# Optimization experiments

Measured on AMD Instinct MI355X. Metric: run time of the kernel, lower is better.

The kernel has to match this reference:

```python
import jax, jax.numpy as jnp
import numpy as np

B, S, H = 1, 2048, 2048
NH, NKV, HD = 32, 4, 128
G = NH // NKV            # query groups per kv head
EPS = 1e-6
THETA = 1000000.0


def _rmsnorm(x, w):
    # per-head RMSNorm over last (head_dim) axis
    var = jnp.mean(jnp.square(x), axis=-1, keepdims=True)
    return x * jax.lax.rsqrt(var + EPS) * w


def _rotate_half(x):
    x1, x2 = jnp.split(x, 2, axis=-1)
    return jnp.concatenate([-x2, x1], axis=-1)


def _rope(x, cos, sin):
    # x: [B,S,h,HD], cos/sin: [S,HD]
    c = cos[None, :, None, :]
    s = sin[None, :, None, :]
    return x * c + _rotate_half(x) * s


def setup_inputs() -> dict:
    key = jax.random.key(0)
    ks = jax.random.split(key, 7)
    inv_freq = 1.0 / (THETA ** (jnp.arange(0, HD, 2, dtype=jnp.float32) / HD))
    freqs = jnp.outer(jnp.arange(S, dtype=jnp.float32), inv_freq)  # [S, HD/2]
    emb = jnp.concatenate([freqs, freqs], axis=-1)                 # [S, HD]
    std = 0.02
    return {
        "hidden_states": jax.random.normal(ks[0], (B, S, H), jnp.float32),
        "wq": jax.random.normal(ks[1], (H, NH * HD), jnp.float32) * std,
        "wk": jax.random.normal(ks[2], (H, NKV * HD), jnp.float32) * std,
        "wv": jax.random.normal(ks[3], (H, NKV * HD), jnp.float32) * std,
        "wo": jax.random.normal(ks[4], (NH * HD, H), jnp.float32) * std,
        "q_norm_w": jnp.ones((HD,), jnp.float32),
        "k_norm_w": jnp.ones((HD,), jnp.float32),
        "cos": jnp.cos(emb),
        "sin": jnp.sin(emb),
    }


def reference(hidden_states, wq, wk, wv, wo, q_norm_w, k_norm_w, cos, sin):
    b, s, _ = hidden_states.shape
    q = (hidden_states @ wq).reshape(b, s, NH, HD)
    k = (hidden_states @ wk).reshape(b, s, NKV, HD)
    v = (hidden_states @ wv).reshape(b, s, NKV, HD)
    # QK per-head RMSNorm, then interleaved RoPE (rotate-half form)
    q = _rope(_rmsnorm(q, q_norm_w), cos, sin)
    k = _rope(_rmsnorm(k, k_norm_w), cos, sin)
    # GQA: group Q heads per KV head instead of materializing repeated K/V
    qg = q.reshape(b, s, NKV, G, HD)
    scaling = HD ** -0.5
    scores = jnp.einsum('bqhgd,bkhd->bhgqk', qg, k) * scaling  # [B,NKV,G,S,S]
    causal = jnp.tril(jnp.ones((s, s), bool))
    scores = jnp.where(causal, scores, jnp.finfo(scores.dtype).min)
    p = jax.nn.softmax(scores, axis=-1)
    attn = jnp.einsum('bhgqk,bkhd->bqhgd', p, v).reshape(b, s, NH * HD)
    return attn @ wo
```

## Files before the change

### kernel.cpp

```cpp
#include <hip/hip_runtime.h>
#include <hip/hip_bf16.h>
#include <stdint.h>

#define SEQ 2048
#define HDIM 128
#define NHEADS 32
#define NKVH 4

typedef unsigned short u16;
typedef __bf16 bf16_t;
typedef bf16_t bf16x8 __attribute__((ext_vector_type(8)));
typedef float floatx4 __attribute__((ext_vector_type(4)));

__device__ __forceinline__ float bf2f(u16 u) {
  union { uint32_t i; float f; } v; v.i = ((uint32_t)u) << 16; return v.f;
}
__device__ __forceinline__ u16 f2bf(float f) {
  if (__builtin_isnan(f)) return 0;
  union { float f; uint32_t i; } v; v.f = f;
  uint32_t r = v.i + 0x7fffu + ((v.i >> 16) & 1u);
  return (u16)(r >> 16);
}
__device__ __forceinline__ float loadf_any(const void* p, size_t i, int isbf) {
  return isbf ? bf2f(((const u16*)p)[i]) : ((const float*)p)[i];
}

__device__ __forceinline__ void gload_lds16(const u16* g, u16* l) {
  __builtin_amdgcn_global_load_lds((__attribute__((address_space(1))) void*)g,
                                   (__attribute__((address_space(3))) void*)l,
                                   16, 0, 0);
}

__device__ __forceinline__ floatx4 mfma16(bf16x8 a, bf16x8 b, floatx4 c) {
  return __builtin_amdgcn_mfma_f32_16x16x32_bf16(a, b, c, 0, 0, 0);
}

struct InPack { const u16* p[9]; int n[9]; };

__global__ void detect_all(InPack pk, int* __restrict__ flags) {
  const int which = blockIdx.x;
  const u16* x = pk.p[which];
  const int n = pk.n[which];
  __shared__ int s_sane, s_zeven, s_zodd;
  if (threadIdx.x == 0) { s_sane = 0; s_zeven = 0; s_zodd = 0; }
  __syncthreads();
  const int ns = n < 8192 ? n : 8192;
  int sane = 0, zeven = 0, zodd = 0;
  for (int i = threadIdx.x; i < ns; i += 256) {
    const u16 u = x[i];
    const int e = (u >> 7) & 0xff;
    if ((e >= 96 && e <= 159) || u == 0) sane++;
    if (u == 0) { if (i & 1) zodd++; else zeven++; }
  }
#pragma unroll
  for (int off = 32; off >= 1; off >>= 1) {
    sane += __shfl_xor(sane, off, 64);
    zeven += __shfl_xor(zeven, off, 64);
    zodd += __shfl_xor(zodd, off, 64);
  }
  if ((threadIdx.x & 63) == 0) {
    atomicAdd(&s_sane, sane);
    atomicAdd(&s_zeven, zeven);
    atomicAdd(&s_zodd, zodd);
  }
  __syncthreads();
  if (threadIdx.x == 0) {
    const int even = (ns + 1) / 2, odd = ns / 2;
    const bool mostly_sane = (s_sane * 10 >= ns * 9);
    const bool fp32_const_pattern = (s_zeven * 2 >= even) && (s_zodd * 10 <= odd);
    flags[which] = (mostly_sane && !fp32_const_pattern) ? 1 : 0;
    if (which == 0) flags[15] = 1;
  }
}

__device__ __forceinline__ void transpose_tile(
    u16 (&tile)[64][65], const void* __restrict__ in, u16* __restrict__ out,
    int R, int C, int isbf, int bx, int by) {
  const int c0 = bx * 64, r0 = by * 64;
  const int t = threadIdx.x;
  const int tr = t >> 4;
  const int tc4 = (t & 15) * 4;
  if (isbf) {
#pragma unroll
    for (int i = 0; i < 4; i++) {
      const int r = i * 16 + tr;
      const ushort4 v = *(const ushort4*)((const u16*)in +
                                          (size_t)(r0 + r) * C + c0 + tc4);
      tile[r][tc4 + 0] = v.x; tile[r][tc4 + 1] = v.y;
      tile[r][tc4 + 2] = v.z; tile[r][tc4 + 3] = v.w;
    }
  } else {
#pragma unroll
    for (int i = 0; i < 4; i++) {
      const int r = i * 16 + tr;
      const float4 v = *(const float4*)((const float*)in +
                                        (size_t)(r0 + r) * C + c0 + tc4);
      tile[r][tc4 + 0] = f2bf(v.x); tile[r][tc4 + 1] = f2bf(v.y);
      tile[r][tc4 + 2] = f2bf(v.z); tile[r][tc4 + 3] = f2bf(v.w);
    }
  }
  __syncthreads();
#pragma unroll
  for (int j = 0; j < 4; j++) {
    const int cc = j * 16 + tr;
    ushort4 o;
    o.x = tile[tc4 + 0][cc]; o.y = tile[tc4 + 1][cc];
    o.z = tile[tc4 + 2][cc]; o.w = tile[tc4 + 3][cc];
    *(ushort4*)(out + (size_t)(c0 + cc) * R + r0 + tc4) = o;
  }
}

__global__ __launch_bounds__(256) void prep_all(
    const void* __restrict__ hs, const void* __restrict__ wq,
    const void* __restrict__ wk, const void* __restrict__ wv,
    u16* __restrict__ Hb, u16* __restrict__ wqkvT,
    const int* __restrict__ flags) {
  __shared__ u16 tile[64][65];
  const int b = blockIdx.x;
  if (b < 2048) {
    transpose_tile(tile, wq, wqkvT, 2048, 4096, flags[1], b & 63, b >> 6);
  } else if (b < 2304) {
    const int r = b - 2048;
    transpose_tile(tile, wk, wqkvT + 4096ull * 2048, 2048, 512, flags[2],
                   r & 7, r >> 3);
  } else if (b < 2560) {
    const int r = b - 2304;
    transpose_tile(tile, wv, wqkvT + 4608ull * 2048, 2048, 512, flags[3],
                   r & 7, r >> 3);
  } else {
    const int r = b - 2560;
    const int base = r * 1024 + threadIdx.x * 4;
    if (flags[0]) {
      *(ushort4*)(Hb + base) = *(const ushort4*)((const u16*)hs + base);
    } else {
      const float4 v = *(const float4*)((const float*)hs + base);
      ushort4 o;
      o.x = f2bf(v.x); o.y = f2bf(v.y); o.z = f2bf(v.z); o.w = f2bf(v.w);
      *(ushort4*)(Hb + base) = o;
    }
  }
}

__global__ __launch_bounds__(256) void transpose_any(
    const void* __restrict__ in, u16* __restrict__ out, int R, int C,
    const int* __restrict__ flag) {
  __shared__ u16 tile[64][65];
  transpose_tile(tile, in, out, R, C, *flag, blockIdx.x, blockIdx.y);
}

__global__ __launch_bounds__(256) void gemm_bt_bf16(
    const u16* __restrict__ A, const u16* __restrict__ BT,
    void* __restrict__ C, int M, int N, int K,
    const int* __restrict__ cflag) {
  __shared__ alignas(16) u16 As[128 * 32];
  __shared__ alignas(16) u16 Bs[128 * 32];
  const int t = threadIdx.x;
  const int w = t >> 6;
  const int lane = t & 63;
  const int lhi = lane >> 4, llo = lane & 15;
  const int m0 = blockIdx.y * 128, n0 = blockIdx.x * 128;
  const int wm = (w & 1) * 64, wn = (w >> 1) * 64;

  floatx4 acc[4][4];
#pragma unroll
  for (int i = 0; i < 4; i++)
#pragma unroll
    for (int j = 0; j < 4; j++) acc[i][j] = (floatx4)(0.0f);

  for (int k0 = 0; k0 < K; k0 += 32) {
#pragma unroll
    for (int r = 0; r < 2; r++) {
      const int c = r * 256 + t;
      const int row = c >> 2, kc = c & 3;
      const int base = (r * 256 + w * 64) * 8;
      gload_lds16(A + (size_t)(m0 + row) * K + k0 + kc * 8, &As[base]);
      gload_lds16(BT + (size_t)(n0 + row) * K + k0 + kc * 8, &Bs[base]);
    }
    __syncthreads();
    bf16x8 af[4], bfr[4];
#pragma unroll
    for (int i = 0; i < 4; i++)
      af[i] = *(const bf16x8*)&As[(wm + i * 16 + llo) * 32 + lhi * 8];
#pragma unroll
    for (int j = 0; j < 4; j++)
      bfr[j] = *(const bf16x8*)&Bs[(wn + j * 16 + llo) * 32 + lhi * 8];
#pragma unroll
    for (int i = 0; i < 4; i++)
#pragma unroll
      for (int j = 0; j < 4; j++)
        acc[i][j] = mfma16(af[i], bfr[j], acc[i][j]);
    __syncthreads();
  }
  const int cbf = *cflag;
#pragma unroll
  for (int i = 0; i < 4; i++) {
    const int row0 = m0 + wm + i * 16 + lhi * 4;
#pragma unroll
    for (int j = 0; j < 4; j++) {
      const int col = n0 + wn + j * 16 + llo;
#pragma unroll
      for (int r = 0; r < 4; r++) {
        if (cbf) ((u16*)C)[(size_t)(row0 + r) * N + col] = f2bf(acc[i][j][r]);
        else ((float*)C)[(size_t)(row0 + r) * N + col] = acc[i][j][r];
      }
    }
  }
}

__global__ __launch_bounds__(1024) void gemm_bt_splitk(
    const u16* __restrict__ A, const u16* __restrict__ BT,
    void* __restrict__ C, int M, int N, int K,
    const int* __restrict__ cflag) {
  __shared__ alignas(16) u16 smem[4][2][128 * 32];
  const int t = threadIdx.x;
  const int g = t >> 8;
  const int tg = t & 255;
  const int w = tg >> 6;
  const int lane = t & 63;
  const int lhi = lane >> 4, llo = lane & 15;
  const int m0 = blockIdx.y * 128, n0 = blockIdx.x * 128;
  const int wm = (w & 1) * 64, wn = (w >> 1) * 64;
  const int kq = K >> 2;
  const int kbeg = g * kq;
  u16* As = smem[g][0];
  u16* Bs = smem[g][1];

  floatx4 acc[4][4];
#pragma unroll
  for (int i = 0; i < 4; i++)
#pragma unroll
    for (int j = 0; j < 4; j++) acc[i][j] = (floatx4)(0.0f);

  for (int k0 = 0; k0 < kq; k0 += 32) {
#pragma unroll
    for (int r = 0; r < 2; r++) {
      const int c = r * 256 + tg;
      const int row = c >> 2, kc = c & 3;
      const int base = (r * 256 + w * 64) * 8;
      gload_lds16(A + (size_t)(m0 + row) * K + kbeg + k0 + kc * 8, &As[base]);
      gload_lds16(BT + (size_t)(n0 + row) * K + kbeg + k0 + kc * 8, &Bs[base]);
    }
    __syncthreads();
    bf16x8 af[4], bfr[4];
#pragma unroll
    for (int i = 0; i < 4; i++)
      af[i] = *(const bf16x8*)&As[(wm + i * 16 + llo) * 32 + lhi * 8];
#pragma unroll
    for (int j = 0; j < 4; j++)
      bfr[j] = *(const bf16x8*)&Bs[(wn + j * 16 + llo) * 32 + lhi * 8];
#pragma unroll
    for (int i = 0; i < 4; i++)
#pragma unroll
      for (int j = 0; j < 4; j++)
        acc[i][j] = mfma16(af[i], bfr[j], acc[i][j]);
    __syncthreads();
  }

  float* red = (float*)&smem[0][0][0];
  for (int gg = 0; gg < 4; gg++) {
    if (g == gg) {
#pragma unroll
      for (int i = 0; i < 4; i++)
#pragma unroll
        for (int j = 0; j < 4; j++) {
          const int col = wn + j * 16 + llo;
#pragma unroll
          for (int r = 0; r < 4; r++) {
            const int row = wm + i * 16 + lhi * 4 + r;
            if (gg == 0) red[row * 128 + col] = acc[i][j][r];
            else red[row * 128 + col] += acc[i][j][r];
          }
        }
    }
    __syncthreads();
  }
  const int cbf = *cflag;
#pragma unroll
  for (int i = 0; i < 16; i++) {
    const int idx = i * 1024 + t;
    const int rr = idx >> 7, cc = idx & 127;
    const float v = red[rr * 128 + cc];
    if (cbf) ((u16*)C)[(size_t)(m0 + rr) * N + n0 + cc] = f2bf(v);
    else ((float*)C)[(size_t)(m0 + rr) * N + n0 + cc] = v;
  }
}

__global__ __launch_bounds__(256) void norm_rope_vt(
    u16* __restrict__ QKV, u16* __restrict__ Vt,
    const void* __restrict__ qw, const void* __restrict__ kw,
    const void* __restrict__ cosb, const void* __restrict__ sinb,
    const int* __restrict__ flags) {
  __shared__ float sw[2][2];
  __shared__ float sh[2][128];
  __shared__ u16 tile[64][65];
  const int b = blockIdx.x;
  const int t = threadIdx.x;
  if (b < 36864) {
    const int qwbf = flags[5], kwbf = flags[6], cbf = flags[7], sbf = flags[8];
    const int s = b / 18, hp = b - s * 18;
    const int g = t >> 7, d = t & 127;
    const int hy = hp * 2 + g;
    const bool isQ = hy < NHEADS;
    const int col = isQ ? hy * HDIM : 4096 + (hy - NHEADS) * HDIM;
    u16* ptr = QKV + (size_t)s * 5120 + col + d;
    const float x = bf2f(*ptr);
    float v = x * x;
#pragma unroll
    for (int off = 32; off >= 1; off >>= 1) v += __shfl_xor(v, off, 64);
    if ((d & 63) == 0) sw[g][d >> 6] = v;
    __syncthreads();
    const float mean = (sw[g][0] + sw[g][1]) * (1.0f / 128.0f);
    const float rn = rsqrtf(mean + 1e-6f);
    const float wv = isQ ? loadf_any(qw, d, qwbf) : loadf_any(kw, d, kwbf);
    const float xn = x * rn * wv;
    sh[g][d] = xn;
    __syncthreads();
    const float other = sh[g][d ^ 64];
    const float cv = loadf_any(cosb, (size_t)s * HDIM + d, cbf);
    const float sv = loadf_any(sinb, (size_t)s * HDIM + d, sbf);
    const float o = xn * cv + (d < 64 ? -other : other) * sv;
    *ptr = f2bf(o);
  } else {
    const int r = b - 36864;
    const int s0 = (r & 31) * 64, d0 = ((r >> 5) & 1) * 64, hk = r >> 6;
#pragma unroll
    for (int i = 0; i < 16; i++) {
      const int idx = i * 256 + t;
      const int rr = idx >> 6, c = idx & 63;
      tile[rr][c] = QKV[(size_t)(s0 + rr) * 5120 + 4608 + hk * HDIM + d0 + c];
    }
    __syncthreads();
#pragma unroll
    for (int i = 0; i < 16; i++) {
      const int idx = i * 256 + t;
      const int dd = idx >> 6, ss = idx & 63;
      Vt[((size_t)hk * HDIM + d0 + dd) * SEQ + s0 + ss] = tile[ss][dd];
    }
  }
}

__global__ __launch_bounds__(256) void flash_attn(
    const u16* __restrict__ QKV, const u16* __restrict__ Vt,
    u16* __restrict__ O) {
  __shared__ alignas(16) u16 Klds[64 * 128];
  __shared__ alignas(16) u16 Vlds[128 * 64];
  __shared__ alignas(16) u16 Plds[4][32 * 72];
  const int t = threadIdx.x;
  const int w = t >> 6;
  const int lane = t & 63;
  const int lhi = lane >> 4, llo = lane & 15;
  const int b = blockIdx.x;
  const int bi = b & 255;
  const int qt = (b < 256) ? (15 - (bi >> 5)) : (bi >> 5);
  const int h = bi & 31, hk = h >> 3;
  const int q0 = qt * 128;
  const int qw0 = q0 + w * 32;
  const float scale = 0.08838834764831845f;
  const float SMAX = 16.0f;

  bf16x8 qf[2][4];
#pragma unroll
  for (int i = 0; i < 2; i++)
#pragma unroll
    for (int c = 0; c < 4; c++)
      qf[i][c] = *(const bf16x8*)(QKV + (size_t)(qw0 + i * 16 + llo) * 5120 +
                                  h * HDIM + c * 32 + lhi * 8);

  floatx4 oacc[2][8];
  float lacc[2][4];
#pragma unroll
  for (int i = 0; i < 2; i++) {
#pragma unroll
    for (int d = 0; d < 8; d++) oacc[i][d] = (floatx4)(0.0f);
#pragma unroll
    for (int r = 0; r < 4; r++) lacc[i][r] = 0.0f;
  }

  const int ntiles = 2 * qt + 2;
  for (int tt = 0; tt < ntiles; tt++) {
    const int kv0 = tt * 64;
#pragma unroll
    for (int r = 0; r < 4; r++) {
      const int c = r * 256 + t;
      const int base = (r * 256 + w * 64) * 8;
      gload_lds16(QKV + (size_t)(kv0 + (c >> 4)) * 5120 + 4096 + hk * HDIM +
                      (((c & 15) ^ ((c >> 4) & 7)) * 8),
                  &Klds[base]);
      gload_lds16(Vt + ((size_t)hk * HDIM + (c >> 3)) * SEQ + kv0 +
                      (((c & 7) ^ ((c >> 3) & 7)) * 8),
                  &Vlds[base]);
    }
    __syncthreads();

    floatx4 sacc[2][4];
#pragma unroll
    for (int i = 0; i < 2; i++)
#pragma unroll
      for (int j = 0; j < 4; j++) sacc[i][j] = (floatx4)(0.0f);
#pragma unroll
    for (int j = 0; j < 4; j++) {
#pragma unroll
      for (int c = 0; c < 4; c++) {
        bf16x8 kf = *(const bf16x8*)&Klds[(j * 16 + llo) * 128 +
                                          (((c * 4 + lhi) ^ (llo & 7)) * 8)];
        sacc[0][j] = mfma16(qf[0][c], kf, sacc[0][j]);
        sacc[1][j] = mfma16(qf[1][c], kf, sacc[1][j]);
      }
    }
    if (kv0 + 64 > q0) {
#pragma unroll
      for (int i = 0; i < 2; i++)
#pragma unroll
        for (int j = 0; j < 4; j++) {
          const int n = kv0 + j * 16 + llo;
#pragma unroll
          for (int r = 0; r < 4; r++) {
            const int mm = qw0 + i * 16 + lhi * 4 + r;
            if (n > mm) sacc[i][j][r] = -30000.0f;
          }
        }
    }
#pragma unroll
    for (int i = 0; i < 2; i++)
#pragma unroll
      for (int j = 0; j < 4; j++)
#pragma unroll
        for (int r = 0; r < 4; r++) {
          const float p = __expf(fmaf(sacc[i][j][r], scale, -SMAX));
          lacc[i][r] += p;
          *(bf16_t*)&Plds[w][(i * 16 + lhi * 4 + r) * 72 + j * 16 + llo] =
              (bf16_t)p;
        }
    asm volatile("" ::: "memory");
    __builtin_amdgcn_s_waitcnt(0);
    asm volatile("" ::: "memory");
#pragma unroll
    for (int c = 0; c < 2; c++) {
      bf16x8 pf0 = *(const bf16x8*)&Plds[w][llo * 72 + c * 32 + lhi * 8];
      bf16x8 pf1 = *(const bf16x8*)&Plds[w][(16 + llo) * 72 + c * 32 + lhi * 8];
#pragma unroll
      for (int d = 0; d < 8; d++) {
        bf16x8 vf = *(const bf16x8*)&Vlds[(d * 16 + llo) * 64 +
                                          (((c * 4 + lhi) ^ (llo & 7)) * 8)];
        oacc[0][d] = mfma16(pf0, vf, oacc[0][d]);
        oacc[1][d] = mfma16(pf1, vf, oacc[1][d]);
      }
    }
    __syncthreads();
  }
#pragma unroll
  for (int i = 0; i < 2; i++)
#pragma unroll
    for (int r = 0; r < 4; r++) {
#pragma unroll
      for (int off = 1; off < 16; off <<= 1)
        lacc[i][r] += __shfl_xor(lacc[i][r], off, 64);
      const float linv = 1.0f / lacc[i][r];
      const int row = qw0 + i * 16 + lhi * 4 + r;
#pragma unroll
      for (int d = 0; d < 8; d++)
        O[(size_t)row * 4096 + h * HDIM + d * 16 + llo] =
            f2bf(oacc[i][d][r] * linv);
    }
}

extern "C" void kernel_launch(void* const* d_in, const int* in_sizes, int n_in,
                              void* d_out, int out_size, void* d_ws, size_t ws_size,
                              hipStream_t stream) {
  char* ws = (char*)d_ws;
  u16* wqkvT  = (u16*)(ws);
  u16* QKVp   = (u16*)(ws + (20ull << 20));
  u16* Vt     = (u16*)(ws + (40ull << 20));
  int* flags  = (int*)(ws + (42ull << 20));
  u16* attnO  = wqkvT;
  u16* woT    = QKVp;
  u16* Hb     = (u16*)d_out;

  InPack pk;
  for (int i = 0; i < 9; i++) { pk.p[i] = (const u16*)d_in[i]; pk.n[i] = in_sizes[i]; }
  detect_all<<<9, 256, 0, stream>>>(pk, flags);

  prep_all<<<6656, 256, 0, stream>>>(
      d_in[0], d_in[1], d_in[2], d_in[3], Hb, wqkvT, flags);

  gemm_bt_bf16<<<dim3(40, 16), 256, 0, stream>>>(
      Hb, wqkvT, QKVp, 2048, 5120, 2048, flags + 15);

  norm_rope_vt<<<37120, 256, 0, stream>>>(
      QKVp, Vt, d_in[5], d_in[6], d_in[7], d_in[8], flags);

  flash_attn<<<512, 256, 0, stream>>>(QKVp, Vt, attnO);

  transpose_any<<<dim3(32, 64), 256, 0, stream>>>(d_in[4], woT, 4096, 2048, flags + 4);
  gemm_bt_splitk<<<dim3(16, 16), 1024, 0, stream>>>(
      attnO, woT, d_out, 2048, 2048, 4096, flags + 0);
}
```

Baseline: 385.8 us.

## Halve flash-attention query tile to 64 rows and fold wo transpose into prep

Flash attention now gives each block 64 query rows (16 per wave) instead of 128, doubling the grid to 1024 blocks. Query tiles are paired so long and short causal tiles are scheduled together for load balance. This raises occupancy and parallelism at the cost of loading each K/V tile for twice as many blocks. Separately, when the workspace is large enough, the wo transpose is merged into the prep_all launch with its own buffer, removing one kernel launch.

Result: faster. 364.9 us (-5.4%).

```diff
diff --git a/kernel.cpp b/kernel.cpp
--- a/kernel.cpp
+++ b/kernel.cpp
@@ -113,8 +113,9 @@
 __global__ __launch_bounds__(256) void prep_all(
     const void* __restrict__ hs, const void* __restrict__ wq,
     const void* __restrict__ wk, const void* __restrict__ wv,
-    u16* __restrict__ Hb, u16* __restrict__ wqkvT,
-    const int* __restrict__ flags) {
+    const void* __restrict__ wo,
+    u16* __restrict__ Hb, u16* __restrict__ wqkvT, u16* __restrict__ woT,
+    int has_wo, const int* __restrict__ flags) {
   __shared__ u16 tile[64][65];
   const int b = blockIdx.x;
   if (b < 2048) {
@@ -127,8 +128,11 @@
     const int r = b - 2304;
     transpose_tile(tile, wv, wqkvT + 4608ull * 2048, 2048, 512, flags[3],
                    r & 7, r >> 3);
+  } else if (has_wo && b < 4608) {
+    const int r = b - 2560;
+    transpose_tile(tile, wo, woT, 4096, 2048, flags[4], r & 31, r >> 5);
   } else {
-    const int r = b - 2560;
+    const int r = b - (has_wo ? 4608 : 2560);
     const int base = r * 1024 + threadIdx.x * 4;
     if (flags[0]) {
       *(ushort4*)(Hb + base) = *(const ushort4*)((const u16*)hs + base);
@@ -344,39 +348,39 @@
     u16* __restrict__ O) {
   __shared__ alignas(16) u16 Klds[64 * 128];
   __shared__ alignas(16) u16 Vlds[128 * 64];
-  __shared__ alignas(16) u16 Plds[4][32 * 72];
+  __shared__ alignas(16) u16 Plds[4][16 * 40];
   const int t = threadIdx.x;
   const int w = t >> 6;
   const int lane = t & 63;
   const int lhi = lane >> 4, llo = lane & 15;
   const int b = blockIdx.x;
   const int bi = b & 255;
-  const int qt = (b < 256) ? (15 - (bi >> 5)) : (bi >> 5);
+  const int kq = bi >> 5;
+  int qt;
+  if (b < 256) qt = 31 - kq;
+  else if (b < 512) qt = kq;
+  else if (b < 768) qt = 23 - kq;
+  else qt = 8 + kq;
   const int h = bi & 31, hk = h >> 3;
-  const int q0 = qt * 128;
-  const int qw0 = q0 + w * 32;
+  const int q0 = qt * 64;
+  const int qw0 = q0 + w * 16;
   const float scale = 0.08838834764831845f;
   const float SMAX = 16.0f;
 
-  bf16x8 qf[2][4];
-#pragma unroll
-  for (int i = 0; i < 2; i++)
-#pragma unroll
-    for (int c = 0; c < 4; c++)
-      qf[i][c] = *(const bf16x8*)(QKV + (size_t)(qw0 + i * 16 + llo) * 5120 +
-                                  h * HDIM + c * 32 + lhi * 8);
-
-  floatx4 oacc[2][8];
-  float lacc[2][4];
-#pragma unroll
-  for (int i = 0; i < 2; i++) {
-#pragma unroll
-    for (int d = 0; d < 8; d++) oacc[i][d] = (floatx4)(0.0f);
-#pragma unroll
-    for (int r = 0; r < 4; r++) lacc[i][r] = 0.0f;
-  }
-
-  const int ntiles = 2 * qt + 2;
+  bf16x8 qf[4];
+#pragma unroll
+  for (int c = 0; c < 4; c++)
+    qf[c] = *(const bf16x8*)(QKV + (size_t)(qw0 + llo) * 5120 +
+                             h * HDIM + c * 32 + lhi * 8);
+
+  floatx4 oacc[8];
+  float lacc[4];
+#pragma unroll
+  for (int d = 0; d < 8; d++) oacc[d] = (floatx4)(0.0f);
+#pragma unroll
+  for (int r = 0; r < 4; r++) lacc[r] = 0.0f;
+
+  const int ntiles = qt + 1;
   for (int tt = 0; tt < ntiles; tt++) {
     const int kv0 = tt * 64;
 #pragma unroll
@@ -392,76 +396,66 @@
     }
     __syncthreads();
 
-    floatx4 sacc[2][4];
-#pragma unroll
-    for (int i = 0; i < 2; i++)
-#pragma unroll
-      for (int j = 0; j < 4; j++) sacc[i][j] = (floatx4)(0.0f);
+    floatx4 sacc[4];
+#pragma unroll
+    for (int j = 0; j < 4; j++) sacc[j] = (floatx4)(0.0f);
 #pragma unroll
     for (int j = 0; j < 4; j++) {
 #pragma unroll
       for (int c = 0; c < 4; c++) {
         bf16x8 kf = *(const bf16x8*)&Klds[(j * 16 + llo) * 128 +
                                           (((c * 4 + lhi) ^ (llo & 7)) * 8)];
-        sacc[0][j] = mfma16(qf[0][c], kf, sacc[0][j]);
-        sacc[1][j] = mfma16(qf[1][c], kf, sacc[1][j]);
+        sacc[j] = mfma16(qf[c], kf, sacc[j]);
       }
     }
     if (kv0 + 64 > q0) {
 #pragma unroll
-      for (int i = 0; i < 2; i++)
-#pragma unroll
-        for (int j = 0; j < 4; j++) {
-          const int n = kv0 + j * 16 + llo;
-#pragma unroll
-          for (int r = 0; r < 4; r++) {
-            const int mm = qw0 + i * 16 + lhi * 4 + r;
-            if (n > mm) sacc[i][j][r] = -30000.0f;
-          }
+      for (int j = 0; j < 4; j++) {
+        const int n = kv0 + j * 16 + llo;
+#pragma unroll
+        for (int r = 0; r < 4; r++) {
+          const int mm = qw0 + lhi * 4 + r;
+          if (n > mm) sacc[j][r] = -30000.0f;
         }
-    }
-#pragma unroll
-    for (int i = 0; i < 2; i++)
-#pragma unroll
-      for (int j = 0; j < 4; j++)
+      }
+    }
+#pragma unroll
+    for (int hh = 0; hh < 2; hh++) {
+#pragma unroll
+      for (int jj = 0; jj < 2; jj++) {
+        const int j = hh * 2 + jj;
 #pragma unroll
         for (int r = 0; r < 4; r++) {
-          const float p = __expf(fmaf(sacc[i][j][r], scale, -SMAX));
-          lacc[i][r] += p;
-          *(bf16_t*)&Plds[w][(i * 16 + lhi * 4 + r) * 72 + j * 16 + llo] =
-              (bf16_t)p;
+          const float p = __expf(fmaf(sacc[j][r], scale, -SMAX));
+          lacc[r] += p;
+          *(bf16_t*)&Plds[w][(lhi * 4 + r) * 40 + jj * 16 + llo] = (bf16_t)p;
         }
-    asm volatile("" ::: "memory");
-    __builtin_amdgcn_s_waitcnt(0);
-    asm volatile("" ::: "memory");
-#pragma unroll
-    for (int c = 0; c < 2; c++) {
-      bf16x8 pf0 = *(const bf16x8*)&Plds[w][llo * 72 + c * 32 + lhi * 8];
-      bf16x8 pf1 = *(const bf16x8*)&Plds[w][(16 + llo) * 72 + c * 32 + lhi * 8];
+      }
+      asm volatile("" ::: "memory");
+      __builtin_amdgcn_s_waitcnt(0);
+      asm volatile("" ::: "memory");
+      bf16x8 pf = *(const bf16x8*)&Plds[w][llo * 40 + lhi * 8];
 #pragma unroll
       for (int d = 0; d < 8; d++) {
         bf16x8 vf = *(const bf16x8*)&Vlds[(d * 16 + llo) * 64 +
-                                          (((c * 4 + lhi) ^ (llo & 7)) * 8)];
-        oacc[0][d] = mfma16(pf0, vf, oacc[0][d]);
-        oacc[1][d] = mfma16(pf1, vf, oacc[1][d]);
+                                          (((hh * 4 + lhi) ^ (llo & 7)) * 8)];
+        oacc[d] = mfma16(pf, vf, oacc[d]);
       }
     }
     __syncthreads();
   }
 #pragma unroll
-  for (int i = 0; i < 2; i++)
-#pragma unroll
-    for (int r = 0; r < 4; r++) {
-#pragma unroll
-      for (int off = 1; off < 16; off <<= 1)
-        lacc[i][r] += __shfl_xor(lacc[i][r], off, 64);
-      const float linv = 1.0f / lacc[i][r];
-      const int row = qw0 + i * 16 + lhi * 4 + r;
-#pragma unroll
-      for (int d = 0; d < 8; d++)
-        O[(size_t)row * 4096 + h * HDIM + d * 16 + llo] =
-            f2bf(oacc[i][d][r] * linv);
-    }
+  for (int r = 0; r < 4; r++) {
+#pragma unroll
+    for (int off = 1; off < 16; off <<= 1)
+      lacc[r] += __shfl_xor(lacc[r], off, 64);
+    const float linv = 1.0f / lacc[r];
+    const int row = qw0 + lhi * 4 + r;
+#pragma unroll
+    for (int d = 0; d < 8; d++)
+      O[(size_t)row * 4096 + h * HDIM + d * 16 + llo] =
+          f2bf(oacc[d][r] * linv);
+  }
 }
 
 extern "C" void kernel_launch(void* const* d_in, const int* in_sizes, int n_in,
@@ -473,15 +467,19 @@
   u16* Vt     = (u16*)(ws + (40ull << 20));
   int* flags  = (int*)(ws + (42ull << 20));
   u16* attnO  = wqkvT;
-  u16* woT    = QKVp;
   u16* Hb     = (u16*)d_out;
+
+  const bool bigws = ws_size >= (61ull << 20);
+  u16* woT = bigws ? (u16*)(ws + (44ull << 20))
+                   : QKVp;
 
   InPack pk;
   for (int i = 0; i < 9; i++) { pk.p[i] = (const u16*)d_in[i]; pk.n[i] = in_sizes[i]; }
   detect_all<<<9, 256, 0, stream>>>(pk, flags);
 
-  prep_all<<<6656, 256, 0, stream>>>(
-      d_in[0], d_in[1], d_in[2], d_in[3], Hb, wqkvT, flags);
+  prep_all<<<bigws ? 8704 : 6656, 256, 0, stream>>>(
+      d_in[0], d_in[1], d_in[2], d_in[3], d_in[4], Hb, wqkvT, woT,
+      bigws ? 1 : 0, flags);
 
   gemm_bt_bf16<<<dim3(40, 16), 256, 0, stream>>>(
       Hb, wqkvT, QKVp, 2048, 5120, 2048, flags + 15);
@@ -489,9 +487,11 @@
   norm_rope_vt<<<37120, 256, 0, stream>>>(
       QKVp, Vt, d_in[5], d_in[6], d_in[7], d_in[8], flags);
 
-  flash_attn<<<512, 256, 0, stream>>>(QKVp, Vt, attnO);
-
-  transpose_any<<<dim3(32, 64), 256, 0, stream>>>(d_in[4], woT, 4096, 2048, flags + 4);
+  flash_attn<<<1024, 256, 0, stream>>>(QKVp, Vt, attnO);
+
+  if (!bigws)
+    transpose_any<<<dim3(32, 64), 256, 0, stream>>>(d_in[4], woT, 4096, 2048,
+                                                    flags + 4);
   gemm_bt_splitk<<<dim3(16, 16), 1024, 0, stream>>>(
       attnO, woT, d_out, 2048, 2048, 4096, flags + 0);
 }
```
